# Performance work log

Measured on AMD Instinct MI355X. Metric: run time of the kernel, lower is better.

Reference implementation:

```python
import jax, jax.numpy as jnp
import numpy as np

B, T, D, H = 256, 256, 64, 512  # batch, seq_len, input_dim, hidden_dim


def setup_inputs() -> dict:
    key = jax.random.key(0)
    ks = jax.random.split(key, 12)
    scale = 0.05
    inp = {"x": jax.random.normal(ks[0], (B, T, D), dtype=jnp.float32)}
    in_dims = [D, H, H]
    for i in range(3):
        inp[f"Wx{i}"] = jax.random.normal(ks[1 + 3 * i], (in_dims[i], H), dtype=jnp.float32) * scale
        inp[f"Wh{i}"] = jax.random.normal(ks[2 + 3 * i], (H, H), dtype=jnp.float32) * scale
        inp[f"b{i}"] = jnp.zeros((H,), dtype=jnp.float32)
    inp["Wf"] = jax.random.normal(ks[10], (H, 1), dtype=jnp.float32) * scale
    inp["bf"] = jnp.zeros((1,), dtype=jnp.float32)
    return inp


def _rnn_seq(x, Wx, Wh, b):
    """SimpleRNN with return_sequences=True. x: [B,T,Din] -> [B,T,H].
    Keras eval mode: dropout inactive. h_t = tanh(x_t Wx + h_{t-1} Wh + b)."""
    # Precompute input projection for all steps (one big GEMM).
    xp = jnp.einsum('btd,dh->bth', x, Wx) + b  # [B,T,H]

    def step(h, xt):
        h2 = jnp.tanh(xt + h @ Wh)
        return h2, h2

    h0 = jnp.zeros((x.shape[0], Wh.shape[0]), dtype=x.dtype)
    _, ys = jax.lax.scan(step, h0, jnp.swapaxes(xp, 0, 1))  # ys: [T,B,H]
    return jnp.swapaxes(ys, 0, 1)


def _rnn_last(x, Wx, Wh, b):
    """SimpleRNN with return_sequences=False. x: [B,T,Din] -> [B,H] (final state)."""
    xp = jnp.einsum('btd,dh->bth', x, Wx) + b

    def step(h, xt):
        h2 = jnp.tanh(xt + h @ Wh)
        return h2, None

    h0 = jnp.zeros((x.shape[0], Wh.shape[0]), dtype=x.dtype)
    hT, _ = jax.lax.scan(step, h0, jnp.swapaxes(xp, 0, 1))
    return hT


def reference(x, Wx0, Wh0, b0, Wx1, Wh1, b1, Wx2, Wh2, b2, Wf, bf):
    h = _rnn_seq(x, Wx0, Wh0, b0)   # [B,T,H]
    h = _rnn_seq(h, Wx1, Wh1, b1)   # [B,T,H]
    h = _rnn_last(h, Wx2, Wh2, b2)  # [B,H]
    return h @ Wf + bf              # [B,1]
```

## Files before the change

### kernel.cpp

```cpp
#include <hip/hip_runtime.h>


typedef unsigned short u16;
typedef unsigned int   u32;

typedef __attribute__((ext_vector_type(8))) short short8;
typedef __attribute__((ext_vector_type(4))) float f32x4;
typedef __attribute__((ext_vector_type(4))) int   i32x4;

#define N_B 256
#define N_T 256
#define N_D 64
#define N_H 512
#define LAY 3
#define BG  8
#define CGS 8
#define ROWS 32
#define WCOL 64
#define CNT_TGT 16
#define HSK_TGT 24
#define CPAD 16
#define CNT_LINES (LAY * BG * N_T)
#define CNT_U32   ((CNT_LINES + 2 * BG) * CPAD)

__device__ __forceinline__ u16 f2bf(float f) {
  union { float f; u32 u; } v; v.f = f;
  u32 u = v.u;
  u += 0x7fffu + ((u >> 16) & 1u);
  return (u16)(u >> 16);
}
__device__ __forceinline__ float bf2f(u16 h) {
  union { u32 u; float f; } v; v.u = ((u32)h) << 16;
  return v.f;
}
__device__ __forceinline__ short8 ld8(const u16* p) { return *(const short8*)p; }
__device__ __forceinline__ short8 cvt8(const float* p) {
  short8 r;
#pragma unroll
  for (int j = 0; j < 8; ++j) r[j] = (short)f2bf(p[j]);
  return r;
}
__device__ __forceinline__ short8 as_s8(i32x4 v) {
  union { i32x4 i; short8 s; } u; u.i = v; return u.s;
}
__device__ __forceinline__ float fast_tanh(float x) {
  float xc = fminf(fmaxf(x, -9.f), 9.f);
  float e  = __builtin_amdgcn_exp2f(xc * 2.8853900817779268f);
  return 1.f - 2.f * __builtin_amdgcn_rcpf(e + 1.f);
}
__device__ __forceinline__ u32 rmw_read(u32* p) {
  u32 v, z = 0;
  asm volatile("global_atomic_add %0, %1, %2, off sc0\n\ts_waitcnt vmcnt(0)"
               : "=v"(v) : "v"(p), "v"(z) : "memory");
  return v;
}

__device__ __forceinline__ void load_frags16_fast(const u16* p, i32x4 f[16]) {
  asm volatile(
      "global_load_dwordx4 %0, %16, off sc0\n\t"
      "global_load_dwordx4 %1, %16, off offset:64 sc0\n\t"
      "global_load_dwordx4 %2, %16, off offset:128 sc0\n\t"
      "global_load_dwordx4 %3, %16, off offset:192 sc0\n\t"
      "global_load_dwordx4 %4, %16, off offset:256 sc0\n\t"
      "global_load_dwordx4 %5, %16, off offset:320 sc0\n\t"
      "global_load_dwordx4 %6, %16, off offset:384 sc0\n\t"
      "global_load_dwordx4 %7, %16, off offset:448 sc0\n\t"
      "global_load_dwordx4 %8, %16, off offset:512 sc0\n\t"
      "global_load_dwordx4 %9, %16, off offset:576 sc0\n\t"
      "global_load_dwordx4 %10, %16, off offset:640 sc0\n\t"
      "global_load_dwordx4 %11, %16, off offset:704 sc0\n\t"
      "global_load_dwordx4 %12, %16, off offset:768 sc0\n\t"
      "global_load_dwordx4 %13, %16, off offset:832 sc0\n\t"
      "global_load_dwordx4 %14, %16, off offset:896 sc0\n\t"
      "global_load_dwordx4 %15, %16, off offset:960 sc0\n\t"
      "s_waitcnt vmcnt(0)"
      : "=&v"(f[0]), "=&v"(f[1]), "=&v"(f[2]), "=&v"(f[3]),
        "=&v"(f[4]), "=&v"(f[5]), "=&v"(f[6]), "=&v"(f[7]),
        "=&v"(f[8]), "=&v"(f[9]), "=&v"(f[10]), "=&v"(f[11]),
        "=&v"(f[12]), "=&v"(f[13]), "=&v"(f[14]), "=&v"(f[15])
      : "v"(p) : "memory");
}
__device__ __forceinline__ void load_frags16_slow(const u16* p, i32x4 f[16]) {
  asm volatile(
      "global_load_dwordx4 %0, %16, off sc0 sc1\n\t"
      "global_load_dwordx4 %1, %16, off offset:64 sc0 sc1\n\t"
      "global_load_dwordx4 %2, %16, off offset:128 sc0 sc1\n\t"
      "global_load_dwordx4 %3, %16, off offset:192 sc0 sc1\n\t"
      "global_load_dwordx4 %4, %16, off offset:256 sc0 sc1\n\t"
      "global_load_dwordx4 %5, %16, off offset:320 sc0 sc1\n\t"
      "global_load_dwordx4 %6, %16, off offset:384 sc0 sc1\n\t"
      "global_load_dwordx4 %7, %16, off offset:448 sc0 sc1\n\t"
      "global_load_dwordx4 %8, %16, off offset:512 sc0 sc1\n\t"
      "global_load_dwordx4 %9, %16, off offset:576 sc0 sc1\n\t"
      "global_load_dwordx4 %10, %16, off offset:640 sc0 sc1\n\t"
      "global_load_dwordx4 %11, %16, off offset:704 sc0 sc1\n\t"
      "global_load_dwordx4 %12, %16, off offset:768 sc0 sc1\n\t"
      "global_load_dwordx4 %13, %16, off offset:832 sc0 sc1\n\t"
      "global_load_dwordx4 %14, %16, off offset:896 sc0 sc1\n\t"
      "global_load_dwordx4 %15, %16, off offset:960 sc0 sc1\n\t"
      "s_waitcnt vmcnt(0)"
      : "=&v"(f[0]), "=&v"(f[1]), "=&v"(f[2]), "=&v"(f[3]),
        "=&v"(f[4]), "=&v"(f[5]), "=&v"(f[6]), "=&v"(f[7]),
        "=&v"(f[8]), "=&v"(f[9]), "=&v"(f[10]), "=&v"(f[11]),
        "=&v"(f[12]), "=&v"(f[13]), "=&v"(f[14]), "=&v"(f[15])
      : "v"(p) : "memory");
}

#define MFMA16(a, b, c) __builtin_amdgcn_mfma_f32_16x16x32_bf16((a), (b), (c), 0, 0, 0)

__global__ __launch_bounds__(256, 1)
void rnn_pipe(const float* __restrict__ x,
              const float* __restrict__ Wx0, const float* __restrict__ Wh0, const float* __restrict__ b0,
              const float* __restrict__ Wx1, const float* __restrict__ Wh1, const float* __restrict__ b1,
              const float* __restrict__ Wx2, const float* __restrict__ Wh2, const float* __restrict__ b2,
              u16* __restrict__ seq0, u16* __restrict__ seq1, u16* __restrict__ seq2,
              u32* __restrict__ cnt) {
  const int b    = blockIdx.x & 7;
  const int rst  = blockIdx.x >> 3;
  const int layer = rst >> 3;
  const int j    = rst & 7;
  const int tid  = threadIdx.x;
  const int lane = tid & 63;
  const int w    = tid >> 6;
  const int quad = lane >> 4;
  const int l16  = lane & 15;
  const int half = w & 1;
  const bool is_rec = (w < 2);

  const float *Wx, *Wh, *bias; const u16 *in_seq = nullptr; u16 *out_seq;
  if (layer == 0)      { Wx = Wx0; Wh = Wh0; bias = b0; out_seq = seq0; }
  else if (layer == 1) { Wx = Wx1; Wh = Wh1; bias = b1; in_seq = seq0; out_seq = seq1; }
  else                 { Wx = Wx2; Wh = Wh2; bias = b2; in_seq = seq1; out_seq = seq2; }
  const int kin = (layer == 0) ? N_D : N_H;
  u32* cnt_own  = cnt + (size_t)(layer * BG + b) * N_T * CPAD;
  u32* cnt_prev = (layer > 0) ? cnt + (size_t)((layer - 1) * BG + b) * N_T * CPAD : nullptr;
  u32* hsk_arr  = cnt + (size_t)(CNT_LINES + b) * CPAD;
  u32* hsk_msk  = cnt + (size_t)(CNT_LINES + BG + b) * CPAD;

  __shared__ u16   WhT[WCOL][N_H];
  __shared__ u16   WxT[WCOL][N_H];
  __shared__ float Cbuf[2][ROWS][WCOL + 1];
  __shared__ u32   fastsh;

  u32 xcc;
  asm volatile("s_getreg_b32 %0, hwreg(HW_REG_XCC_ID)" : "=s"(xcc));
  if (tid == 0) {
    __hip_atomic_fetch_or(hsk_msk, 1u << (xcc & 7), __ATOMIC_RELAXED,
                          __HIP_MEMORY_SCOPE_AGENT);
    asm volatile("s_waitcnt vmcnt(0)" ::: "memory");
    __hip_atomic_fetch_add(hsk_arr, 1u, __ATOMIC_RELAXED, __HIP_MEMORY_SCOPE_AGENT);
  }

  for (int e = tid; e < WCOL * N_H; e += 256) {
    int n = e & 63, k = e >> 6;
    WhT[n][(k + 8 * n) & (N_H - 1)] = f2bf(Wh[k * N_H + j * WCOL + n]);
  }
  for (int e = tid; e < WCOL * kin; e += 256) {
    int n = e & 63, k = e >> 6;
    WxT[n][(k + 8 * n) & (kin - 1)] = f2bf(Wx[k * N_H + j * WCOL + n]);
  }
  float bv[4];
#pragma unroll
  for (int n = 0; n < 4; ++n) bv[n] = bias[j * WCOL + n * 16 + l16];

  if (tid == 0) {
    bool f = false;
    u32 it = 0;
    while (rmw_read(hsk_arr) < (u32)HSK_TGT) {
      __builtin_amdgcn_s_sleep(1);
      if (++it > (1u << 22)) break;
    }
    if (it <= (1u << 22)) {
      u32 m = rmw_read(hsk_msk);
      f = (m != 0u) && ((m & (m - 1u)) == 0u);
    }
    fastsh = f ? 1u : 0u;
  }
  __syncthreads();
  const bool fast = (fastsh == 1u);

  const int arow = b * ROWS + half * 16 + l16;
  bool dead = false;

  for (int t = 0; t < N_T; ++t) {
    const int par = t & 1;
    f32x4 acc[4] = {{0.f,0.f,0.f,0.f},{0.f,0.f,0.f,0.f},{0.f,0.f,0.f,0.f},{0.f,0.f,0.f,0.f}};

    if (!is_rec) {
      if (layer == 0) {
        const float* xp = x + ((size_t)arow * N_T + t) * N_D + quad * 8;
        short8 f0 = cvt8(xp), f1 = cvt8(xp + 32);
#pragma unroll
        for (int n = 0; n < 4; ++n) {
          int nl = n * 16 + l16;
          acc[n] = MFMA16(f0, ld8(&WxT[nl][(quad * 8 + 8 * nl) & (N_D - 1)]), acc[n]);
          acc[n] = MFMA16(f1, ld8(&WxT[nl][(32 + quad * 8 + 8 * nl) & (N_D - 1)]), acc[n]);
        }
      } else {
        if (lane == 0 && !dead) {
          u32* cp = cnt_prev + (size_t)t * CPAD;
          u32 it = 0;
          for (;;) {
            u32 v = fast ? rmw_read(cp)
                         : __hip_atomic_load(cp, __ATOMIC_RELAXED, __HIP_MEMORY_SCOPE_AGENT);
            if (v >= (u32)CNT_TGT) break;
            __builtin_amdgcn_s_sleep(1);
            if (++it > (1u << 22)) { dead = true; break; }
          }
        }
        const u16* sp = in_seq + ((size_t)t * N_B + arow) * N_H + quad * 8;
        i32x4 fr[16];
        if (fast) load_frags16_fast(sp, fr);
        else      load_frags16_slow(sp, fr);
#pragma unroll
        for (int kt = 0; kt < 16; ++kt) {
          short8 a = as_s8(fr[kt]);
#pragma unroll
          for (int n = 0; n < 4; ++n) {
            int nl = n * 16 + l16;
            acc[n] = MFMA16(a, ld8(&WxT[nl][(kt * 32 + quad * 8 + 8 * nl) & (N_H - 1)]), acc[n]);
          }
        }
      }
      int rb = half * 16 + quad * 4;
#pragma unroll
      for (int n = 0; n < 4; ++n)
#pragma unroll
        for (int r = 0; r < 4; ++r)
          Cbuf[par][rb + r][n * 16 + l16] = acc[n][r];
    } else {
      if (t > 0) {
        if (lane == 0 && !dead) {
          u32* cp = cnt_own + (size_t)(t - 1) * CPAD;
          u32 it = 0;
          for (;;) {
            u32 v = fast ? rmw_read(cp)
                         : __hip_atomic_load(cp, __ATOMIC_RELAXED, __HIP_MEMORY_SCOPE_AGENT);
            if (v >= (u32)CNT_TGT) break;
            __builtin_amdgcn_s_sleep(1);
            if (++it > (1u << 22)) { dead = true; break; }
          }
        }
        const u16* ap = out_seq + ((size_t)(t - 1) * N_B + arow) * N_H + quad * 8;
        i32x4 fr[16];
        if (fast) load_frags16_fast(ap, fr);
        else      load_frags16_slow(ap, fr);
#pragma unroll
        for (int kt = 0; kt < 16; ++kt) {
          short8 a = as_s8(fr[kt]);
#pragma unroll
          for (int n = 0; n < 4; ++n) {
            int nl = n * 16 + l16;
            acc[n] = MFMA16(a, ld8(&WhT[nl][(kt * 32 + quad * 8 + 8 * nl) & (N_H - 1)]), acc[n]);
          }
        }
      }
    }

    __syncthreads();

    if (is_rec) {
      int rb = half * 16 + quad * 4;
      u32 hv[4][4];
#pragma unroll
      for (int n = 0; n < 4; ++n)
#pragma unroll
        for (int r = 0; r < 4; ++r)
          hv[n][r] = (u32)f2bf(fast_tanh(acc[n][r] + Cbuf[par][rb + r][n * 16 + l16] + bv[n]));
      u16* hdst = out_seq + ((size_t)t * N_B + b * ROWS + half * 16 + quad * 4) * N_H
                  + j * WCOL + l16;
      if (fast) {
        asm volatile(
            "global_store_short %0, %1, off sc0\n\t"
            "global_store_short %0, %2, off offset:1024 sc0\n\t"
            "global_store_short %0, %3, off offset:2048 sc0\n\t"
            "global_store_short %0, %4, off offset:3072 sc0\n\t"
            "global_store_short %0, %5, off offset:32 sc0\n\t"
            "global_store_short %0, %6, off offset:1056 sc0\n\t"
            "global_store_short %0, %7, off offset:2080 sc0\n\t"
            "global_store_short %0, %8, off offset:3104 sc0\n\t"
            "global_store_short %0, %9, off offset:64 sc0\n\t"
            "global_store_short %0, %10, off offset:1088 sc0\n\t"
            "global_store_short %0, %11, off offset:2112 sc0\n\t"
            "global_store_short %0, %12, off offset:3136 sc0\n\t"
            "global_store_short %0, %13, off offset:96 sc0\n\t"
            "global_store_short %0, %14, off offset:1120 sc0\n\t"
            "global_store_short %0, %15, off offset:2144 sc0\n\t"
            "global_store_short %0, %16, off offset:3168 sc0"
            :: "v"(hdst),
               "v"(hv[0][0]), "v"(hv[0][1]), "v"(hv[0][2]), "v"(hv[0][3]),
               "v"(hv[1][0]), "v"(hv[1][1]), "v"(hv[1][2]), "v"(hv[1][3]),
               "v"(hv[2][0]), "v"(hv[2][1]), "v"(hv[2][2]), "v"(hv[2][3]),
               "v"(hv[3][0]), "v"(hv[3][1]), "v"(hv[3][2]), "v"(hv[3][3])
            : "memory");
      } else {
        asm volatile(
            "global_store_short %0, %1, off sc0 sc1\n\t"
            "global_store_short %0, %2, off offset:1024 sc0 sc1\n\t"
            "global_store_short %0, %3, off offset:2048 sc0 sc1\n\t"
            "global_store_short %0, %4, off offset:3072 sc0 sc1\n\t"
            "global_store_short %0, %5, off offset:32 sc0 sc1\n\t"
            "global_store_short %0, %6, off offset:1056 sc0 sc1\n\t"
            "global_store_short %0, %7, off offset:2080 sc0 sc1\n\t"
            "global_store_short %0, %8, off offset:3104 sc0 sc1\n\t"
            "global_store_short %0, %9, off offset:64 sc0 sc1\n\t"
            "global_store_short %0, %10, off offset:1088 sc0 sc1\n\t"
            "global_store_short %0, %11, off offset:2112 sc0 sc1\n\t"
            "global_store_short %0, %12, off offset:3136 sc0 sc1\n\t"
            "global_store_short %0, %13, off offset:96 sc0 sc1\n\t"
            "global_store_short %0, %14, off offset:1120 sc0 sc1\n\t"
            "global_store_short %0, %15, off offset:2144 sc0 sc1\n\t"
            "global_store_short %0, %16, off offset:3168 sc0 sc1"
            :: "v"(hdst),
               "v"(hv[0][0]), "v"(hv[0][1]), "v"(hv[0][2]), "v"(hv[0][3]),
               "v"(hv[1][0]), "v"(hv[1][1]), "v"(hv[1][2]), "v"(hv[1][3]),
               "v"(hv[2][0]), "v"(hv[2][1]), "v"(hv[2][2]), "v"(hv[2][3]),
               "v"(hv[3][0]), "v"(hv[3][1]), "v"(hv[3][2]), "v"(hv[3][3])
            : "memory");
      }
      asm volatile("s_waitcnt vmcnt(0)" ::: "memory");
      if (lane == 0) {
        u32* cp = cnt_own + (size_t)t * CPAD;
        if (fast) {
          u32 one = 1u;
          asm volatile("global_atomic_add %0, %1, off" :: "v"(cp), "v"(one) : "memory");
        } else {
          __hip_atomic_fetch_add(cp, 1u, __ATOMIC_RELAXED, __HIP_MEMORY_SCOPE_AGENT);
        }
      }
    }
  }
}

__global__ void head_kernel(const u16* __restrict__ seq2, const float* __restrict__ Wf,
                            const float* __restrict__ bf, float* __restrict__ out) {
  int b    = blockIdx.x;
  int lane = threadIdx.x;
  const u16* hrow = seq2 + ((size_t)(N_T - 1) * N_B + b) * N_H;
  float s = 0.f;
#pragma unroll
  for (int r = 0; r < N_H / 64; ++r) {
    int idx = lane * 8 + r;
    s += bf2f(hrow[idx]) * Wf[idx];
  }
#pragma unroll
  for (int off = 32; off > 0; off >>= 1) s += __shfl_down(s, off);
  if (lane == 0) out[b] = s + bf[0];
}

extern "C" void kernel_launch(void* const* d_in, const int* in_sizes, int n_in,
                              void* d_out, int out_size, void* d_ws, size_t ws_size,
                              hipStream_t stream) {
  const float* x   = (const float*)d_in[0];
  const float* Wx0 = (const float*)d_in[1];
  const float* Wh0 = (const float*)d_in[2];
  const float* b0  = (const float*)d_in[3];
  const float* Wx1 = (const float*)d_in[4];
  const float* Wh1 = (const float*)d_in[5];
  const float* b1  = (const float*)d_in[6];
  const float* Wx2 = (const float*)d_in[7];
  const float* Wh2 = (const float*)d_in[8];
  const float* b2  = (const float*)d_in[9];
  const float* Wf  = (const float*)d_in[10];
  const float* bf  = (const float*)d_in[11];
  float* out = (float*)d_out;

  const size_t SEQ_BYTES = (size_t)N_T * N_B * N_H * sizeof(u16);
  if (ws_size < 3 * SEQ_BYTES + (size_t)CNT_U32 * sizeof(u32)) return;

  char* ws  = (char*)d_ws;
  u16* seq0 = (u16*)(ws);
  u16* seq1 = (u16*)(ws + SEQ_BYTES);
  u16* seq2 = (u16*)(ws + 2 * SEQ_BYTES);
  u32* cnt  = (u32*)(ws + 3 * SEQ_BYTES);

  (void)hipMemsetAsync(cnt, 0, (size_t)CNT_U32 * sizeof(u32), stream);

  rnn_pipe<<<LAY * BG * CGS, 256, 0, stream>>>(x, Wx0, Wh0, b0, Wx1, Wh1, b1,
                                               Wx2, Wh2, b2, seq0, seq1, seq2,
                                               cnt);
  head_kernel<<<N_B, 64, 0, stream>>>(seq2, Wf, bf, out);
}
```

Before: 1.232 ms.

## Poll global counters from one wave per pair and relay via LDS flags

Only the half-0 wave of each wave pair now polls the global step counter and publishes readiness to its partner through LDS flags. On output, the half-1 wave signals through LDS, and only half 0 issues the global atomic increment. This halves both the number of arrivals per step (the target drops from 16 to 8) and the global polling traffic. Spinning in the first two poll iterations no longer sleeps, which cuts wake-up latency. The risk is extra intra-workgroup handoff latency, and the LDS flag protocol must order the partner wave's global stores correctly.

After: 1.218 ms. No clear change (-1.1%).

```diff
diff --git a/kernel.cpp b/kernel.cpp
--- a/kernel.cpp
+++ b/kernel.cpp
@@ -17,11 +17,12 @@
 #define CGS 8
 #define ROWS 32
 #define WCOL 64
-#define CNT_TGT 16
+#define CNT_TGT 8
 #define HSK_TGT 24
 #define CPAD 16
 #define CNT_LINES (LAY * BG * N_T)
 #define CNT_U32   ((CNT_LINES + 2 * BG) * CPAD)
+#define SPIN_LIM (1u << 22)
 
 __device__ __forceinline__ u16 f2bf(float f) {
   union { float f; u32 u; } v; v.f = f;
@@ -53,6 +54,25 @@
   asm volatile("global_atomic_add %0, %1, %2, off sc0\n\ts_waitcnt vmcnt(0)"
                : "=v"(v) : "v"(p), "v"(z) : "memory");
   return v;
+}
+__device__ __forceinline__ void poll_cnt(u32* cp, u32 target, bool fast, bool* dead) {
+  u32 it = 0;
+  for (;;) {
+    u32 v = fast ? rmw_read(cp)
+                 : __hip_atomic_load(cp, __ATOMIC_RELAXED, __HIP_MEMORY_SCOPE_AGENT);
+    if (v >= target) return;
+    if (it >= 2) __builtin_amdgcn_s_sleep(1);
+    if (++it > SPIN_LIM) { *dead = true; return; }
+  }
+}
+__device__ __forceinline__ void lds_set(volatile u32* f, u32 v) {
+  __hip_atomic_store((u32*)f, v, __ATOMIC_RELEASE, __HIP_MEMORY_SCOPE_WORKGROUP);
+}
+__device__ __forceinline__ void lds_wait(volatile u32* f, u32 want, bool* dead) {
+  u32 it = 0;
+  while (__hip_atomic_load((u32*)f, __ATOMIC_ACQUIRE, __HIP_MEMORY_SCOPE_WORKGROUP) != want) {
+    if (++it > SPIN_LIM) { *dead = true; return; }
+  }
 }
 
 __device__ __forceinline__ void load_frags16_fast(const u16* p, i32x4 f[16]) {
@@ -141,6 +161,7 @@
   __shared__ u16   WxT[WCOL][N_H];
   __shared__ float Cbuf[2][ROWS][WCOL + 1];
   __shared__ u32   fastsh;
+  __shared__ u32   sflags[6];
 
   u32 xcc;
   asm volatile("s_getreg_b32 %0, hwreg(HW_REG_XCC_ID)" : "=s"(xcc));
@@ -150,6 +171,7 @@
     asm volatile("s_waitcnt vmcnt(0)" ::: "memory");
     __hip_atomic_fetch_add(hsk_arr, 1u, __ATOMIC_RELAXED, __HIP_MEMORY_SCOPE_AGENT);
   }
+  if (tid < 6) sflags[tid] = 0;
 
   for (int e = tid; e < WCOL * N_H; e += 256) {
     int n = e & 63, k = e >> 6;
@@ -168,9 +190,9 @@
     u32 it = 0;
     while (rmw_read(hsk_arr) < (u32)HSK_TGT) {
       __builtin_amdgcn_s_sleep(1);
-      if (++it > (1u << 22)) break;
+      if (++it > SPIN_LIM) break;
     }
-    if (it <= (1u << 22)) {
+    if (it <= SPIN_LIM) {
       u32 m = rmw_read(hsk_msk);
       f = (m != 0u) && ((m & (m - 1u)) == 0u);
     }
@@ -197,16 +219,13 @@
           acc[n] = MFMA16(f1, ld8(&WxT[nl][(32 + quad * 8 + 8 * nl) & (N_D - 1)]), acc[n]);
         }
       } else {
-        if (lane == 0 && !dead) {
-          u32* cp = cnt_prev + (size_t)t * CPAD;
-          u32 it = 0;
-          for (;;) {
-            u32 v = fast ? rmw_read(cp)
-                         : __hip_atomic_load(cp, __ATOMIC_RELAXED, __HIP_MEMORY_SCOPE_AGENT);
-            if (v >= (u32)CNT_TGT) break;
-            __builtin_amdgcn_s_sleep(1);
-            if (++it > (1u << 22)) { dead = true; break; }
+        if (half == 0) {
+          if (lane == 0) {
+            if (!dead) poll_cnt(cnt_prev + (size_t)t * CPAD, CNT_TGT, fast, &dead);
+            lds_set(&sflags[2 + par], (u32)(t + 1));
           }
+        } else {
+          if (lane == 0 && !dead) lds_wait(&sflags[2 + par], (u32)(t + 1), &dead);
         }
         const u16* sp = in_seq + ((size_t)t * N_B + arow) * N_H + quad * 8;
         i32x4 fr[16];
@@ -230,16 +249,13 @@
           Cbuf[par][rb + r][n * 16 + l16] = acc[n][r];
     } else {
       if (t > 0) {
-        if (lane == 0 && !dead) {
-          u32* cp = cnt_own + (size_t)(t - 1) * CPAD;
-          u32 it = 0;
-          for (;;) {
-            u32 v = fast ? rmw_read(cp)
-                         : __hip_atomic_load(cp, __ATOMIC_RELAXED, __HIP_MEMORY_SCOPE_AGENT);
-            if (v >= (u32)CNT_TGT) break;
-            __builtin_amdgcn_s_sleep(1);
-            if (++it > (1u << 22)) { dead = true; break; }
+        if (half == 0) {
+          if (lane == 0) {
+            if (!dead) poll_cnt(cnt_own + (size_t)(t - 1) * CPAD, CNT_TGT, fast, &dead);
+            lds_set(&sflags[par], (u32)t);
           }
+        } else {
+          if (lane == 0 && !dead) lds_wait(&sflags[par], (u32)t, &dead);
         }
         const u16* ap = out_seq + ((size_t)(t - 1) * N_B + arow) * N_H + quad * 8;
         i32x4 fr[16];
@@ -319,13 +335,18 @@
             : "memory");
       }
       asm volatile("s_waitcnt vmcnt(0)" ::: "memory");
-      if (lane == 0) {
-        u32* cp = cnt_own + (size_t)t * CPAD;
-        if (fast) {
-          u32 one = 1u;
-          asm volatile("global_atomic_add %0, %1, off" :: "v"(cp), "v"(one) : "memory");
-        } else {
-          __hip_atomic_fetch_add(cp, 1u, __ATOMIC_RELAXED, __HIP_MEMORY_SCOPE_AGENT);
+      if (half == 1) {
+        if (lane == 0) lds_set(&sflags[4 + par], (u32)(t + 1));
+      } else {
+        if (lane == 0) {
+          if (!dead) lds_wait(&sflags[4 + par], (u32)(t + 1), &dead);
+          u32* cp = cnt_own + (size_t)t * CPAD;
+          if (fast) {
+            u32 one = 1u;
+            asm volatile("global_atomic_add %0, %1, off" :: "v"(cp), "v"(one) : "memory");
+          } else {
+            __hip_atomic_fetch_add(cp, 1u, __ATOMIC_RELAXED, __HIP_MEMORY_SCOPE_AGENT);
+          }
         }
       }
     }
```
